# Performance work log

Measured on AMD Instinct MI355X. Metric: run time of the kernel, lower is better.

Reference implementation:

```python
import jax, jax.numpy as jnp
from jax import lax
import numpy as np

B, T, H, C = 64, 512, 1024, 21


def setup_inputs() -> dict:
    key = jax.random.key(0)
    k1, k2, k3, k4 = jax.random.split(key, 4)
    return {
        "sequence_output": jax.random.normal(k1, (B, T, H), dtype=jnp.float32),
        "input_mask": jax.random.randint(k2, (B, T), 0, 2, dtype=jnp.int32),
        "W": jax.random.normal(k3, (H, C), dtype=jnp.float32) * 0.02,
        "b": jnp.zeros((C,), dtype=jnp.float32),
        "transitions": jax.random.normal(k4, (C, C), dtype=jnp.float32) * 0.1,
    }


def crf_decode(logits, transitions, seq_len):
    """Viterbi decode matching tfa.text.crf_decode semantics (length-masked)."""
    Bb, Tt, Cc = logits.shape
    ident = jnp.arange(Cc, dtype=jnp.int32)[None, :]  # identity backpointers

    def fwd_step(state, inp):
        logit_t, t = inp  # [B,C], scalar step index
        scores = state[:, :, None] + transitions[None, :, :]  # [B, C_prev, C_cur]
        bp = jnp.argmax(scores, axis=1).astype(jnp.int32)      # [B, C]
        new_state = jnp.max(scores, axis=1) + logit_t          # [B, C]
        valid = (t < seq_len)[:, None]                          # [B, 1]
        state = jnp.where(valid, new_state, state)
        bp = jnp.where(valid, bp, ident)
        return state, bp

    ts = jnp.arange(1, Tt)
    xs = (jnp.transpose(logits[:, 1:], (1, 0, 2)), ts)
    final_state, bps = lax.scan(fwd_step, logits[:, 0], xs)  # bps: [T-1, B, C]
    last_tag = jnp.argmax(final_state, axis=-1).astype(jnp.int32)  # [B]

    def back_step(tag, bp_t):
        tag = jnp.take_along_axis(bp_t, tag[:, None], axis=1)[:, 0]
        return tag, tag

    _, tags_rev = lax.scan(back_step, last_tag, bps, reverse=True)  # [T-1, B]
    tags = jnp.concatenate([tags_rev, last_tag[None, :]], axis=0)   # [T, B]
    return jnp.transpose(tags, (1, 0))  # [B, T]


def reference(sequence_output, input_mask, W, b, transitions):
    # classifier logits
    logits = jnp.einsum("bth,hc->btc", sequence_output, W) + b  # [B,T,C]
    mask = (input_mask == 1).astype(jnp.int32)
    seq_len = jnp.sum(mask, axis=-1)  # [B]
    decode_tags = crf_decode(logits, transitions, seq_len)
    return jax.nn.one_hot(decode_tags, logits.shape[-1], dtype=jnp.float32), logits
```

## Files before the change

kernel.cpp:

```cpp
#include <hip/hip_runtime.h>
#include <stdint.h>

#define BB 64
#define TT 512
#define HH 1024
#define CC 21

#define GAS __attribute__((address_space(1)))
#define LAS __attribute__((address_space(3)))
__device__ __forceinline__ void gll16(const void* g, void* l) {
    __builtin_amdgcn_global_load_lds((const GAS uint32_t*)g, (LAS uint32_t*)l, 16, 0, 0);
}

#define RL(x, lane) __uint_as_float(__builtin_amdgcn_readlane(__float_as_uint(x), (lane)))

__global__ __launch_bounds__(256) void logits_kernel(
    const float* __restrict__ seq,
    const float* __restrict__ W,
    const float* __restrict__ bias,
    float* __restrict__ logits)
{
    __shared__ float4 xs[4][2][256];
    __shared__ float  wt[4][2][16 * 24];

    const int t = threadIdx.x;
    const int w = t >> 6;
    const int l = t & 63;
    const int row0 = blockIdx.x * 64;
    const int hbase = w * 256;

    float acc[CC];
#pragma unroll
    for (int c = 0; c < CC; ++c) acc[c] = 0.f;

    float4 xr[4];
    float  wr[6];

    auto issue = [&](int ch) {
        const int h0 = hbase + ch * 16;
#pragma unroll
        for (int k = 0; k < 4; ++k) {
            int r = 16 * k + (l >> 2), s = l & 3;
            xr[k] = *(const float4*)(seq + (size_t)(row0 + r) * HH + h0 + s * 4);
        }
        const float* wg = W + (size_t)h0 * CC;
#pragma unroll
        for (int i = 0; i < 6; ++i) {
            int j = i * 64 + l;
            wr[i] = (j < 16 * CC) ? wg[j] : 0.f;
        }
    };

    auto commit = [&](int buf) {
#pragma unroll
        for (int k = 0; k < 4; ++k)
            xs[w][buf][(l & 3) * 64 + 16 * k + (l >> 2)] = xr[k];
#pragma unroll
        for (int i = 0; i < 6; ++i) {
            int j = i * 64 + l;
            if (j < 16 * CC) wt[w][buf][(j / CC) * 24 + (j % CC)] = wr[i];
        }
    };

    auto compute = [&](int buf) {
        const float4* xb = xs[w][buf];
        const float*  wb = wt[w][buf];
#pragma unroll
        for (int g = 0; g < 4; ++g) {
            float4 xv = xb[g * 64 + l];
#pragma unroll
            for (int j = 0; j < 4; ++j) {
                const float4* wrow = (const float4*)(wb + (g * 4 + j) * 24);
                float xc = (&xv.x)[j];
#pragma unroll
                for (int r5 = 0; r5 < 6; ++r5) {
                    float4 w4 = wrow[r5];
                    int c0 = r5 * 4;
                    acc[c0] += xc * w4.x;
                    if (c0 + 1 < CC) acc[c0 + 1] += xc * w4.y;
                    if (c0 + 2 < CC) acc[c0 + 2] += xc * w4.z;
                    if (c0 + 3 < CC) acc[c0 + 3] += xc * w4.w;
                }
            }
        }
    };

    issue(0);
    commit(0);
    int buf = 0;
#pragma unroll 1
    for (int ch = 0; ch < 16; ++ch) {
        if (ch < 15) issue(ch + 1);
        compute(buf);
        if (ch < 15) commit(buf ^ 1);
        buf ^= 1;
    }

    __syncthreads();
    float* comb = (float*)&xs[0][0][0];
    if (w > 0) {
        float* cr = comb + ((w - 1) * 64 + l) * 22;
#pragma unroll
        for (int c = 0; c < CC; ++c) cr[c] = acc[c];
    }
    __syncthreads();
    if (w == 0) {
        const float* p0 = comb + (size_t)l * 22;
        const float* p1 = comb + (size_t)(64 + l) * 22;
        const float* p2 = comb + (size_t)(128 + l) * 22;
        float* orow = logits + (size_t)(row0 + l) * CC;
#pragma unroll
        for (int c = 0; c < CC; ++c)
            orow[c] = acc[c] + p0[c] + p1[c] + p2[c] + bias[c];
    }
}

__global__ __launch_bounds__(256) void viterbi_kernel(
    const float* __restrict__ logits,
    const int* __restrict__ mask,
    const float* __restrict__ trans,
    float* __restrict__ onehot)
{
    __shared__ __align__(16) float lg[(TT + 1) * CC];
    __shared__ float stS[TT * CC];
    __shared__ float trL[CC * CC];
    __shared__ unsigned char bp[TT * CC];
    __shared__ unsigned char tagl[TT];
    __shared__ unsigned char mapl[8 * CC];
    __shared__ unsigned char bnd[9];

    const int tid = threadIdx.x;
    const int w = tid >> 6;
    const int l = tid & 63;
    const int b = blockIdx.x;

    const float* lb = logits + (size_t)b * TT * CC;
    for (int i = w; i < 42; i += 4)
        gll16(lb + (size_t)(i * 64 + l) * 4, &lg[i * 256]);

    for (int j = tid; j < CC * CC; j += 256) trL[j] = trans[j];

    int sl = 0;
#pragma unroll
    for (int k = 0; k < 8; ++k) sl += mask[b * TT + k * 64 + l];
#pragma unroll
    for (int o = 32; o > 0; o >>= 1) sl += __shfl_xor(sl, o);
    const int idstart = (sl >= 1) ? (sl - 1) : 0;

    asm volatile("s_waitcnt vmcnt(0)" ::: "memory");
    __syncthreads();

    if (w == 0) {
        const bool act = (l < CC);
        const int cc = act ? l : 0;
        float tcol[CC];
#pragma unroll
        for (int cp = 0; cp < CC; ++cp) tcol[cp] = trL[cp * CC + cc];

        float st = lg[cc];
        if (act) stS[l] = st;
        float lgt_next = lg[CC + cc];

#pragma unroll 1
        for (int t = 1; t < sl; ++t) {
            float lgt = lgt_next;
            lgt_next = lg[(t + 1) * CC + cc];
            float sc[CC];
#pragma unroll
            for (int cp = 0; cp < CC; ++cp) sc[cp] = RL(st, cp) + tcol[cp];
            float m0 = fmaxf(fmaxf(sc[0], sc[1]), sc[2]);
            float m1 = fmaxf(fmaxf(sc[3], sc[4]), sc[5]);
            float m2 = fmaxf(fmaxf(sc[6], sc[7]), sc[8]);
            float m3 = fmaxf(fmaxf(sc[9], sc[10]), sc[11]);
            float m4 = fmaxf(fmaxf(sc[12], sc[13]), sc[14]);
            float m5 = fmaxf(fmaxf(sc[15], sc[16]), sc[17]);
            float m6 = fmaxf(fmaxf(sc[18], sc[19]), sc[20]);
            float n0 = fmaxf(fmaxf(m0, m1), m2);
            float n1 = fmaxf(fmaxf(m3, m4), m5);
            float best = fmaxf(fmaxf(n0, n1), m6);
            st = best + lgt;
            if (act) stS[t * CC + l] = st;
        }

        float fs[CC];
#pragma unroll
        for (int cp = 0; cp < CC; ++cp) fs[cp] = RL(st, cp);
        float q0 = fmaxf(fmaxf(fs[0], fs[1]), fs[2]);
        float q1 = fmaxf(fmaxf(fs[3], fs[4]), fs[5]);
        float q2 = fmaxf(fmaxf(fs[6], fs[7]), fs[8]);
        float q3 = fmaxf(fmaxf(fs[9], fs[10]), fs[11]);
        float q4 = fmaxf(fmaxf(fs[12], fs[13]), fs[14]);
        float q5 = fmaxf(fmaxf(fs[15], fs[16]), fs[17]);
        float q6 = fmaxf(fmaxf(fs[18], fs[19]), fs[20]);
        float fbest = fmaxf(fmaxf(fmaxf(q0, q1), fmaxf(q2, q3)),
                            fmaxf(fmaxf(q4, q5), q6));
        int e[CC];
#pragma unroll
        for (int cp = 0; cp < CC; ++cp) e[cp] = (fs[cp] == fbest) ? cp : 63;
        int i0 = min(min(e[0], e[1]), e[2]);
        int i1 = min(min(e[3], e[4]), e[5]);
        int i2 = min(min(e[6], e[7]), e[8]);
        int i3 = min(min(e[9], e[10]), e[11]);
        int i4 = min(min(e[12], e[13]), e[14]);
        int i5 = min(min(e[15], e[16]), e[17]);
        int i6 = min(min(e[18], e[19]), e[20]);
        int last = min(min(min(i0, i1), min(i2, i3)), min(min(i4, i5), i6));
        if (l == 0) tagl[TT - 1] = (unsigned char)last;
    } else {
        int s = (w - 1) * 64 + l;
        if (s < 189) {
            int c0 = s % CC, prow = s / CC;
#pragma unroll 1
            for (int p = idstart + prow; p < TT; p += 9)
                bp[p * CC + c0] = (unsigned char)c0;
        }
    }
    __syncthreads();

    if (tid < 252) {
        const int c0 = tid % CC, tg = tid / CC;
        float tc[CC];
#pragma unroll
        for (int cp = 0; cp < CC; ++cp) tc[cp] = trL[cp * CC + c0];
#pragma unroll 1
        for (int t = 1 + tg; t < sl; t += 12) {
            const float* sp = stS + (t - 1) * CC;
            float bv = sp[0] + tc[0];
            int bi = 0;
#pragma unroll
            for (int cp = 1; cp < CC; ++cp) {
                float v = sp[cp] + tc[cp];
                bool g = v > bv;
                bv = g ? v : bv;
                bi = g ? cp : bi;
            }
            bp[(t - 1) * CC + c0] = (unsigned char)bi;
        }
    }
    __syncthreads();

    if (tid < 168) {
        int g = tid / CC, cand = tid % CC;
        int startp = (g == 7) ? (TT - 2) : (64 * g + 63);
        int endp = 64 * g;
        int m = cand;
#pragma unroll 1
        for (int i = 0; i < 64; ++i) {
            int p = startp - i;
            int pr = (p >= endp) ? p : endp;
            int m2 = bp[pr * CC + m];
            m = (p >= endp) ? m2 : m;
        }
        mapl[g * CC + cand] = (unsigned char)m;
    }
    __syncthreads();

    if (tid == 0) {
        int eb = tagl[TT - 1];
        bnd[8] = (unsigned char)eb;
        for (int g = 7; g >= 0; --g) {
            eb = mapl[g * CC + eb];
            bnd[g] = (unsigned char)eb;
        }
    }
    __syncthreads();

    if (tid < 8) {
        int g = tid;
        int startp = (g == 7) ? (TT - 2) : (64 * g + 63);
        int endp = 64 * g;
        int eb = bnd[g + 1];
#pragma unroll 1
        for (int p = startp; p >= endp; --p) {
            eb = bp[p * CC + eb];
            tagl[p] = (unsigned char)eb;
        }
    }
    __syncthreads();

    if (tid < 252) {
        const int c0 = tid % CC, prow = tid / CC;
        float* ob = onehot + (size_t)b * TT * CC;
#pragma unroll 1
        for (int p = prow; p < TT; p += 12)
            ob[(size_t)p * CC + c0] = (c0 == (int)tagl[p]) ? 1.f : 0.f;
    }
}

extern "C" void kernel_launch(void* const* d_in, const int* in_sizes, int n_in,
                              void* d_out, int out_size, void* d_ws, size_t ws_size,
                              hipStream_t stream) {
    const float* seq   = (const float*)d_in[0];
    const int*   msk   = (const int*)d_in[1];
    const float* W     = (const float*)d_in[2];
    const float* bias  = (const float*)d_in[3];
    const float* trans = (const float*)d_in[4];

    float* onehot_out = (float*)d_out;
    float* logits_out = onehot_out + (size_t)BB * TT * CC;

    logits_kernel<<<512, 256, 0, stream>>>(seq, W, bias, logits_out);
    viterbi_kernel<<<BB, 256, 0, stream>>>(logits_out, msk, trans, onehot_out);
}
```

Baseline: 149.4 us.

## Stream logits inputs via global_load_lds triple buffer and widen Viterbi backtrack segments

The logits GEMM kernel now loads activation chunks straight into LDS with global_load_lds into a three-deep ring buffer, instead of staging them through registers and transposing on store. Manual vmcnt waits let the chunk two steps ahead keep loading while the current one is computed, which is meant to hide global load latency and remove the register-to-LDS copy. The Viterbi backtrack is split into 12 segments of 43 steps instead of 8 of 64, so more threads share the work and each serial chain is shorter. The hand-written vmcnt counts and the missing barriers around the LDS ring buffer rely on each wave touching only its own buffers and on the order in which loads complete.

```diff
diff --git a/kernel.cpp b/kernel.cpp
--- a/kernel.cpp
+++ b/kernel.cpp
@@ -20,58 +20,56 @@
     const float* __restrict__ bias,
     float* __restrict__ logits)
 {
-    __shared__ float4 xs[4][2][256];
-    __shared__ float  wt[4][2][16 * 24];
+    __shared__ __align__(16) float4 xsh[4][3][256];
+    __shared__ __align__(16) float  wsh[4][2][16*24];
 
     const int t = threadIdx.x;
     const int w = t >> 6;
     const int l = t & 63;
     const int row0 = blockIdx.x * 64;
     const int hbase = w * 256;
+    const float* seqrow = seq + (size_t)(row0 + l) * HH + hbase;
 
     float acc[CC];
 #pragma unroll
     for (int c = 0; c < CC; ++c) acc[c] = 0.f;
 
-    float4 xr[4];
-    float  wr[6];
-
-    auto issue = [&](int ch) {
-        const int h0 = hbase + ch * 16;
-#pragma unroll
-        for (int k = 0; k < 4; ++k) {
-            int r = 16 * k + (l >> 2), s = l & 3;
-            xr[k] = *(const float4*)(seq + (size_t)(row0 + r) * HH + h0 + s * 4);
-        }
-        const float* wg = W + (size_t)h0 * CC;
+    float wr[6];
+
+    auto issueX = [&](int ch) {
+        float4* dst = xsh[w][ch % 3];
+#pragma unroll
+        for (int it = 0; it < 4; ++it)
+            gll16(seqrow + ch * 16 + it * 4, dst + it * 64);
+    };
+    auto issueW = [&](int ch) {
+        const float* wg = W + (size_t)(hbase + ch * 16) * CC;
 #pragma unroll
         for (int i = 0; i < 6; ++i) {
             int j = i * 64 + l;
             wr[i] = (j < 16 * CC) ? wg[j] : 0.f;
         }
     };
-
-    auto commit = [&](int buf) {
-#pragma unroll
-        for (int k = 0; k < 4; ++k)
-            xs[w][buf][(l & 3) * 64 + 16 * k + (l >> 2)] = xr[k];
+    auto commitW = [&](int ch) {
+        float* wb = wsh[w][ch & 1];
 #pragma unroll
         for (int i = 0; i < 6; ++i) {
             int j = i * 64 + l;
-            if (j < 16 * CC) wt[w][buf][(j / CC) * 24 + (j % CC)] = wr[i];
+            if (j < 16 * CC) wb[(j / CC) * 24 + (j % CC)] = wr[i];
         }
     };
-
-    auto compute = [&](int buf) {
-        const float4* xb = xs[w][buf];
-        const float*  wb = wt[w][buf];
-#pragma unroll
-        for (int g = 0; g < 4; ++g) {
-            float4 xv = xb[g * 64 + l];
+    auto compute = [&](int ch) {
+        const float4* xb = xsh[w][ch % 3];
+        const float*  wb = wsh[w][ch & 1];
+        float4 xq[4];
+#pragma unroll
+        for (int q = 0; q < 4; ++q) xq[q] = xb[q * 64 + l];
+#pragma unroll
+        for (int q = 0; q < 4; ++q) {
 #pragma unroll
             for (int j = 0; j < 4; ++j) {
-                const float4* wrow = (const float4*)(wb + (g * 4 + j) * 24);
-                float xc = (&xv.x)[j];
+                const float4* wrow = (const float4*)(wb + (q * 4 + j) * 24);
+                float xc = (&xq[q].x)[j];
 #pragma unroll
                 for (int r5 = 0; r5 < 6; ++r5) {
                     float4 w4 = wrow[r5];
@@ -85,19 +83,28 @@
         }
     };
 
-    issue(0);
-    commit(0);
-    int buf = 0;
-#pragma unroll 1
-    for (int ch = 0; ch < 16; ++ch) {
-        if (ch < 15) issue(ch + 1);
-        compute(buf);
-        if (ch < 15) commit(buf ^ 1);
-        buf ^= 1;
-    }
-
-    __syncthreads();
-    float* comb = (float*)&xs[0][0][0];
+    issueX(0);
+    issueW(0);
+    issueX(1);
+    asm volatile("s_waitcnt vmcnt(4)" ::: "memory");
+    commitW(0);
+
+#pragma unroll 1
+    for (int ch = 0; ch < 14; ++ch) {
+        issueW(ch + 1);
+        issueX(ch + 2);
+        compute(ch);
+        asm volatile("s_waitcnt vmcnt(4)" ::: "memory");
+        commitW(ch + 1);
+    }
+    issueW(15);
+    compute(14);
+    asm volatile("s_waitcnt vmcnt(0)" ::: "memory");
+    commitW(15);
+    compute(15);
+
+    __syncthreads();
+    float* comb = (float*)&xsh[0][0][0];
     if (w > 0) {
         float* cr = comb + ((w - 1) * 64 + l) * 22;
 #pragma unroll
@@ -126,8 +133,8 @@
     __shared__ float trL[CC * CC];
     __shared__ unsigned char bp[TT * CC];
     __shared__ unsigned char tagl[TT];
-    __shared__ unsigned char mapl[8 * CC];
-    __shared__ unsigned char bnd[9];
+    __shared__ unsigned char mapl[12 * CC];
+    __shared__ unsigned char bnd[13];
 
     const int tid = threadIdx.x;
     const int w = tid >> 6;
@@ -239,13 +246,13 @@
     }
     __syncthreads();
 
-    if (tid < 168) {
+    if (tid < 252) {
         int g = tid / CC, cand = tid % CC;
-        int startp = (g == 7) ? (TT - 2) : (64 * g + 63);
-        int endp = 64 * g;
+        int endp = g * 43;
+        int startp = min(g * 43 + 42, TT - 2);
         int m = cand;
 #pragma unroll 1
-        for (int i = 0; i < 64; ++i) {
+        for (int i = 0; i < 43; ++i) {
             int p = startp - i;
             int pr = (p >= endp) ? p : endp;
             int m2 = bp[pr * CC + m];
@@ -257,18 +264,18 @@
 
     if (tid == 0) {
         int eb = tagl[TT - 1];
-        bnd[8] = (unsigned char)eb;
-        for (int g = 7; g >= 0; --g) {
+        bnd[12] = (unsigned char)eb;
+        for (int g = 11; g >= 0; --g) {
             eb = mapl[g * CC + eb];
             bnd[g] = (unsigned char)eb;
         }
     }
     __syncthreads();
 
-    if (tid < 8) {
+    if (tid < 12) {
         int g = tid;
-        int startp = (g == 7) ? (TT - 2) : (64 * g + 63);
-        int endp = 64 * g;
+        int endp = g * 43;
+        int startp = min(g * 43 + 42, TT - 2);
         int eb = bnd[g + 1];
 #pragma unroll 1
         for (int p = startp; p >= endp; --p) {
```

After: 131.3 us. 12.1% less time.
